# Optimization experiments

Hardware: AMD Instinct MI355X
Metric: run time of the kernel (lower is better)

Reference implementation:

```python
import jax, jax.numpy as jnp
import numpy as np

B, IN_CH, HID, H, W = 8, 64, 128, 128, 128
WS, NHEADS = 4, 4
HD = HID // NHEADS
GROUPS = 8  # min(8, hidden_ch)
EPS = 1e-5


def setup_inputs() -> dict:
    key = jax.random.key(0)
    ks = jax.random.split(key, 8)
    def w(k, shape):
        return jax.random.normal(k, shape, jnp.float32) * 0.02
    return {
        "x": jax.random.normal(ks[0], (B, IN_CH, H, W), jnp.float32),
        "h": jax.random.normal(ks[1], (B, HID, H, W), jnp.float32),
        "c": jax.random.normal(ks[2], (B, HID, H, W), jnp.float32),
        "Wproj": w(ks[3], (HID, IN_CH + HID)),
        "bproj": jnp.zeros((HID,), jnp.float32),
        "ln_g": jnp.ones((HID,), jnp.float32),
        "ln_b": jnp.zeros((HID,), jnp.float32),
        "Wqkv": w(ks[4], (3 * HID, HID)),
        "bqkv": jnp.zeros((3 * HID,), jnp.float32),
        "Wo": w(ks[5], (HID, HID)),
        "bo": jnp.zeros((HID,), jnp.float32),
        "Wgates": w(ks[6], (4 * HID, HID)),
        "bgates": jnp.zeros((4 * HID,), jnp.float32),
        "gn_g": jnp.ones((HID,), jnp.float32),
        "gn_b": jnp.zeros((HID,), jnp.float32),
    }


def group_norm(x, g, b):
    # x: [B, C, H, W], normalize per (group, spatial)
    Bx, C, Hx, Wx = x.shape
    xg = x.reshape(Bx, GROUPS, C // GROUPS, Hx, Wx)
    mu = xg.mean(axis=(2, 3, 4), keepdims=True)
    var = xg.var(axis=(2, 3, 4), keepdims=True)
    xn = ((xg - mu) * jax.lax.rsqrt(var + EPS)).reshape(Bx, C, Hx, Wx)
    return xn * g[:, None, None] + b[:, None, None]


def reference(x, h, c, Wproj, bproj, ln_g, ln_b, Wqkv, bqkv, Wo, bo,
              Wgates, bgates, gn_g, gn_b):
    # 1x1 conv input projection on concat(x, h)
    comb = jnp.concatenate([x, h], axis=1)  # [B, in+hid, H, W]
    proj = jnp.einsum('bihw,oi->bohw', comb, Wproj) + bproj[:, None, None]

    # window partition (H, W divisible by WS -> no padding)
    nh, nw = H // WS, W // WS
    xw = proj.reshape(B, HID, nh, WS, nw, WS)
    xw = xw.transpose(0, 2, 4, 3, 5, 1).reshape(B * nh * nw, WS * WS, HID)

    # LocalWindowAttention: LayerNorm -> QKV -> MHSA -> proj
    mu = xw.mean(axis=-1, keepdims=True)
    var = xw.var(axis=-1, keepdims=True)
    xn = (xw - mu) * jax.lax.rsqrt(var + EPS) * ln_g + ln_b
    qkv = (xn @ Wqkv.T + bqkv).reshape(-1, WS * WS, 3, NHEADS, HD)
    q = qkv[:, :, 0].transpose(0, 2, 1, 3)  # [Bw, nh, N, hd]
    k = qkv[:, :, 1].transpose(0, 2, 1, 3)
    v = qkv[:, :, 2].transpose(0, 2, 1, 3)
    scale = HD ** -0.5
    attn = jax.nn.softmax(jnp.einsum('whnd,whmd->whnm', q, k) * scale, axis=-1)
    out = jnp.einsum('whnm,whmd->whnd', attn, v)
    out = out.transpose(0, 2, 1, 3).reshape(-1, WS * WS, HID)
    out = out @ Wo.T + bo

    # window unpartition -> [B, C, H, W]
    attn_map = out.reshape(B, nh, nw, WS, WS, HID)
    attn_map = attn_map.transpose(0, 5, 1, 3, 2, 4).reshape(B, HID, H, W)
    attn_map = group_norm(attn_map, gn_g, gn_b)

    # conv-gated LSTM update (1x1 conv gates)
    gates = jnp.einsum('bchw,oc->bohw', attn_map, Wgates) + bgates[:, None, None]
    ci, cf, co, cg = jnp.split(gates, 4, axis=1)
    i = jax.nn.sigmoid(ci)
    f = jax.nn.sigmoid(cf)
    o = jax.nn.sigmoid(co)
    g = jnp.tanh(cg)
    cnext = f * c + i * g
    hnext = group_norm(o * jnp.tanh(cnext), gn_g, gn_b)
    return hnext, cnext
```

## Files before the change

### kernel.cpp

```cpp
#include <hip/hip_runtime.h>
#include <math.h>

typedef unsigned int uint;
typedef unsigned short ushort;
typedef short s16x8 __attribute__((ext_vector_type(8)));
typedef float f32x4 __attribute__((ext_vector_type(4)));

#define PIX 16384
#define EPSF 1e-5f

__device__ __forceinline__ ushort f2bf(float f) {
  union { float f; uint u; } v; v.f = f;
  uint u = v.u;
  uint r = (u + 0x7FFFu + ((u >> 16) & 1u)) >> 16;
  return (ushort)r;
}
__device__ __forceinline__ float bf2f(ushort h) {
  union { uint u; float f; } v; v.u = ((uint)h) << 16;
  return v.f;
}
__device__ __forceinline__ uint pk2(float a, float b) {
  return (uint)f2bf(a) | ((uint)f2bf(b) << 16);
}
__device__ __forceinline__ float fsigmoid(float v) { return 1.f / (1.f + __expf(-v)); }
__device__ __forceinline__ float ftanh(float v) { return 1.f - 2.f / (__expf(2.f * v) + 1.f); }

union Frag { uint4 u4; uint u[4]; s16x8 s; };

__global__ void k_prep(const float* __restrict__ Wp, const float* __restrict__ Wq,
                       const float* __restrict__ Wo, const float* __restrict__ Wg,
                       const float* __restrict__ ln_g,
                       ushort* __restrict__ FWp, ushort* __restrict__ FWq,
                       ushort* __restrict__ FWo, ushort* __restrict__ FWg) {
  int idx = blockIdx.x * 256 + threadIdx.x;
  const float* W; ushort* F; int KS, ldw, rel; bool scale = false;
  if (idx < 3072)       { W = Wp; F = FWp; KS = 6; ldw = 192; rel = idx; }
  else if (idx < 9216)  { W = Wq; F = FWq; KS = 4; ldw = 128; rel = idx - 3072; scale = true; }
  else if (idx < 11264) { W = Wo; F = FWo; KS = 4; ldw = 128; rel = idx - 9216; }
  else                  { W = Wg; F = FWg; KS = 4; ldw = 128; rel = idx - 11264; }
  int l = rel & 63, rest = rel >> 6;
  int ks = rest % KS, mt = rest / KS;
  int col = ks * 32 + (l >> 4) * 8;
  const float* src = W + (size_t)(mt * 16 + (l & 15)) * ldw + col;
  float g[8] = {1.f, 1.f, 1.f, 1.f, 1.f, 1.f, 1.f, 1.f};
  if (scale) {
    #pragma unroll
    for (int j = 0; j < 8; j++) g[j] = ln_g[col + j];
  }
  uint4 v;
  v.x = pk2(src[0] * g[0], src[1] * g[1]);
  v.y = pk2(src[2] * g[2], src[3] * g[3]);
  v.z = pk2(src[4] * g[4], src[5] * g[5]);
  v.w = pk2(src[6] * g[6], src[7] * g[7]);
  *reinterpret_cast<uint4*>(F + (size_t)rel * 8) = v;
}

__global__ void k_prep2(const float* __restrict__ Wq, const float* __restrict__ ln_g,
                        const float* __restrict__ ln_b, const float* __restrict__ bqkv,
                        float* __restrict__ Sarr, float* __restrict__ Tbarr) {
  int o = threadIdx.x;
  if (o >= 384) return;
  float S = 0.f, T = 0.f;
  const float* wr = Wq + (size_t)o * 128;
  for (int i = 0; i < 128; i++) {
    float wv = wr[i];
    S = fmaf(wv, ln_g[i], S);
    T = fmaf(wv, ln_b[i], T);
  }
  Sarr[o] = S;
  Tbarr[o] = T + bqkv[o];
}

__global__ __launch_bounds__(256, 3) void k_attn(
    const float* __restrict__ x, const float* __restrict__ h,
    const ushort* __restrict__ FWp, const float* __restrict__ bproj,
    const ushort* __restrict__ FWq, const float* __restrict__ Sarr,
    const float* __restrict__ Tbarr,
    const ushort* __restrict__ FWoT, const float* __restrict__ bo,
    ushort* __restrict__ attn_map, float* __restrict__ stA_raw)
{
  __shared__ __align__(16) char LM[51200];
  __shared__ float sSum[64], sSum2[64];
  __shared__ float sStat[16];

  const int t = threadIdx.x;
  const int bid = blockIdx.x;
  const int b = bid >> 8, wh = (bid >> 3) & 31, ww0 = bid & 7;
  const int w = t >> 6, l = t & 63, q = l >> 4, r16 = l & 15;

  uint* sInP = (uint*)LM;
  ushort* sXn = (ushort*)LM;

  if (t < 64) { sSum[t] = 0.f; sSum2[t] = 0.f; }
  if (t < 16) sStat[t] = 0.f;

  {
    const float* xb = x + (size_t)b * 64 * PIX;
    const float* hb = h + (size_t)b * 128 * PIX;
    #pragma unroll
    for (int it = 0; it < 6; it++) {
      int item = it * 256 + t;
      int wv = item & 3, r = (item >> 2) & 3, chp = item >> 4;
      int ch0 = chp * 2;
      int gpix = (wh * 4 + r) * 128 + ww0 * 16 + wv * 4;
      float4 a, c2;
      if (ch0 < 64) {
        a  = *reinterpret_cast<const float4*>(xb + (size_t)ch0 * PIX + gpix);
        c2 = *reinterpret_cast<const float4*>(xb + (size_t)(ch0 + 1) * PIX + gpix);
      } else {
        a  = *reinterpret_cast<const float4*>(hb + (size_t)(ch0 - 64) * PIX + gpix);
        c2 = *reinterpret_cast<const float4*>(hb + (size_t)(ch0 - 63) * PIX + gpix);
      }
      uint4 pkd;
      pkd.x = pk2(a.x, c2.x); pkd.y = pk2(a.y, c2.y);
      pkd.z = pk2(a.z, c2.z); pkd.w = pk2(a.w, c2.w);
      *reinterpret_cast<uint4*>(sInP + chp * 68 + wv * 16 + r * 4) = pkd;
    }
  }
  __syncthreads();

  f32x4 acc1[2][4];
  {
    #pragma unroll
    for (int mi = 0; mi < 2; mi++)
      #pragma unroll
      for (int nt = 0; nt < 4; nt++) acc1[mi][nt] = (f32x4){0.f, 0.f, 0.f, 0.f};
    for (int ks = 0; ks < 6; ks++) {
      Frag bf[4];
      #pragma unroll
      for (int nt = 0; nt < 4; nt++)
        #pragma unroll
        for (int s = 0; s < 4; s++)
          bf[nt].u[s] = sInP[(ks * 16 + q * 4 + s) * 68 + nt * 16 + r16];
      #pragma unroll
      for (int mi = 0; mi < 2; mi++) {
        Frag af;
        af.u4 = *reinterpret_cast<const uint4*>(FWp + (((w + mi * 4) * 6 + ks) * 64 + l) * 8);
        #pragma unroll
        for (int nt = 0; nt < 4; nt++)
          acc1[mi][nt] = __builtin_amdgcn_mfma_f32_16x16x32_bf16(af.s, bf[nt].s, acc1[mi][nt], 0, 0, 0);
      }
    }
  }
  __syncthreads();

  {
    float pst[4] = {0.f, 0.f, 0.f, 0.f}, pst2[4] = {0.f, 0.f, 0.f, 0.f};
    #pragma unroll
    for (int mi = 0; mi < 2; mi++) {
      int o0 = (w + mi * 4) * 16 + q * 4;
      const float4 bv = *reinterpret_cast<const float4*>(bproj + o0);
      #pragma unroll
      for (int nt = 0; nt < 4; nt++) {
        float v0 = acc1[mi][nt][0] + bv.x, v1 = acc1[mi][nt][1] + bv.y;
        float v2 = acc1[mi][nt][2] + bv.z, v3 = acc1[mi][nt][3] + bv.w;
        uint2 pk; pk.x = pk2(v0, v1); pk.y = pk2(v2, v3);
        *reinterpret_cast<uint2*>(sXn + (nt * 16 + r16) * 136 + o0) = pk;
        pst[nt]  += v0 + v1 + v2 + v3;
        pst2[nt] += v0 * v0 + v1 * v1 + v2 * v2 + v3 * v3;
      }
    }
    #pragma unroll
    for (int nt = 0; nt < 4; nt++) {
      float s = pst[nt], s2 = pst2[nt];
      s  += __shfl_xor(s, 16);  s  += __shfl_xor(s, 32);
      s2 += __shfl_xor(s2, 16); s2 += __shfl_xor(s2, 32);
      if (q == 0) {
        atomicAdd(&sSum[nt * 16 + r16], s);
        atomicAdd(&sSum2[nt * 16 + r16], s2);
      }
    }
  }
  __syncthreads();

  float rstd_[4], mr_[4];
  f32x4 accV[2][4];
  {
    Frag bfh[4][4];
    #pragma unroll
    for (int ks = 0; ks < 4; ks++)
      #pragma unroll
      for (int nt = 0; nt < 4; nt++)
        bfh[ks][nt].u4 = *reinterpret_cast<const uint4*>(sXn + (nt * 16 + r16) * 136 + ks * 32 + q * 8);

    #pragma unroll
    for (int nt = 0; nt < 4; nt++) {
      int tok = nt * 16 + r16;
      float mu = sSum[tok] * 0.0078125f;
      float var = sSum2[tok] * 0.0078125f - mu * mu;
      rstd_[nt] = rsqrtf(var + EPSF);
      mr_[nt] = -mu * rstd_[nt];
    }

    ushort* sQKu = (ushort*)(LM + 17408);
    #pragma unroll
    for (int mi = 0; mi < 4; mi++) {
      int mt = w + mi * 4;
      f32x4 accq[4];
      #pragma unroll
      for (int nt = 0; nt < 4; nt++) accq[nt] = (f32x4){0.f, 0.f, 0.f, 0.f};
      #pragma unroll
      for (int ks = 0; ks < 4; ks++) {
        Frag af;
        af.u4 = *reinterpret_cast<const uint4*>(FWq + ((mt * 4 + ks) * 64 + l) * 8);
        #pragma unroll
        for (int nt = 0; nt < 4; nt++)
          accq[nt] = __builtin_amdgcn_mfma_f32_16x16x32_bf16(af.s, bfh[ks][nt].s, accq[nt], 0, 0, 0);
      }
      int oo = mt * 16 + q * 4;
      const float4 S4  = *reinterpret_cast<const float4*>(Sarr + oo);
      const float4 Tb4 = *reinterpret_cast<const float4*>(Tbarr + oo);
      #pragma unroll
      for (int nt = 0; nt < 4; nt++) {
        float v0 = fmaf(rstd_[nt], accq[nt][0], fmaf(mr_[nt], S4.x, Tb4.x));
        float v1 = fmaf(rstd_[nt], accq[nt][1], fmaf(mr_[nt], S4.y, Tb4.y));
        float v2 = fmaf(rstd_[nt], accq[nt][2], fmaf(mr_[nt], S4.z, Tb4.z));
        float v3 = fmaf(rstd_[nt], accq[nt][3], fmaf(mr_[nt], S4.w, Tb4.w));
        uint2 pk; pk.x = pk2(v0, v1); pk.y = pk2(v2, v3);
        *reinterpret_cast<uint2*>(sQKu + nt * 4224 + r16 * 264 + oo) = pk;
      }
    }
    #pragma unroll
    for (int mi = 0; mi < 2; mi++) {
      int mt = w + 16 + mi * 4;
      #pragma unroll
      for (int nt = 0; nt < 4; nt++) accV[mi][nt] = (f32x4){0.f, 0.f, 0.f, 0.f};
      #pragma unroll
      for (int ks = 0; ks < 4; ks++) {
        Frag af;
        af.u4 = *reinterpret_cast<const uint4*>(FWq + ((mt * 4 + ks) * 64 + l) * 8);
        #pragma unroll
        for (int nt = 0; nt < 4; nt++)
          accV[mi][nt] = __builtin_amdgcn_mfma_f32_16x16x32_bf16(af.s, bfh[ks][nt].s, accV[mi][nt], 0, 0, 0);
      }
    }
  }
  __syncthreads();

  {
    ushort* sVu = (ushort*)LM;
    #pragma unroll
    for (int mi = 0; mi < 2; mi++) {
      int mt = w + 16 + mi * 4;
      int oo = mt * 16 + q * 4;
      const float4 S4  = *reinterpret_cast<const float4*>(Sarr + oo);
      const float4 Tb4 = *reinterpret_cast<const float4*>(Tbarr + oo);
      #pragma unroll
      for (int nt = 0; nt < 4; nt++) {
        float v0 = fmaf(rstd_[nt], accV[mi][nt][0], fmaf(mr_[nt], S4.x, Tb4.x));
        float v1 = fmaf(rstd_[nt], accV[mi][nt][1], fmaf(mr_[nt], S4.y, Tb4.y));
        float v2 = fmaf(rstd_[nt], accV[mi][nt][2], fmaf(mr_[nt], S4.z, Tb4.z));
        float v3 = fmaf(rstd_[nt], accV[mi][nt][3], fmaf(mr_[nt], S4.w, Tb4.w));
        ushort* vd = sVu + nt * 2048 + (oo - 256) * 16 + r16;
        vd[0] = f2bf(v0); vd[16] = f2bf(v1); vd[32] = f2bf(v2); vd[48] = f2bf(v3);
      }
    }
  }
  __syncthreads();

  {
    const float scale = 0.17677669529663687f;
    ushort* sQKw = (ushort*)(LM + 17408 + w * 8448);
    ushort* sPw  = sQKw;
    Frag af4[4], bf4[4];
    #pragma unroll
    for (int hd = 0; hd < 4; hd++) {
      af4[hd].u4 = *reinterpret_cast<const uint4*>(sQKw + r16 * 264 + hd * 32 + q * 8);
      bf4[hd].u4 = *reinterpret_cast<const uint4*>(sQKw + r16 * 264 + 128 + hd * 32 + q * 8);
    }
    #pragma unroll
    for (int hd = 0; hd < 4; hd++) {
      if (l < 32) {
        int row = l >> 1, hz = l & 1;
        uint4 z = {0u, 0u, 0u, 0u};
        *reinterpret_cast<uint4*>(sPw + hd * 512 + row * 32 + 16 + hz * 8) = z;
      }
    }
    f32x4 sc[4];
    #pragma unroll
    for (int hd = 0; hd < 4; hd++) {
      f32x4 z4 = (f32x4){0.f, 0.f, 0.f, 0.f};
      sc[hd] = __builtin_amdgcn_mfma_f32_16x16x32_bf16(af4[hd].s, bf4[hd].s, z4, 0, 0, 0);
    }
    #pragma unroll
    for (int hd = 0; hd < 4; hd++) {
      ushort* pd = sPw + hd * 512 + (q * 4) * 32 + r16;
      #pragma unroll
      for (int r = 0; r < 4; r++) {
        float sv = sc[hd][r] * scale;
        float mx = sv;
        mx = fmaxf(mx, __shfl_xor(mx, 1));
        mx = fmaxf(mx, __shfl_xor(mx, 2));
        mx = fmaxf(mx, __shfl_xor(mx, 4));
        mx = fmaxf(mx, __shfl_xor(mx, 8));
        float e = __expf(sv - mx);
        float sm = e;
        sm += __shfl_xor(sm, 1); sm += __shfl_xor(sm, 2);
        sm += __shfl_xor(sm, 4); sm += __shfl_xor(sm, 8);
        pd[r * 32] = f2bf(e / sm);
      }
    }
    ushort* sOw = sQKw + 2048;
    ushort* sVw = (ushort*)LM + w * 2048;
    #pragma unroll
    for (int hd = 0; hd < 4; hd++) {
      Frag pa;
      pa.u4 = *reinterpret_cast<const uint4*>(sPw + hd * 512 + r16 * 32 + q * 8);
      #pragma unroll
      for (int nt2 = 0; nt2 < 2; nt2++) {
        int ch = hd * 32 + nt2 * 16 + r16;
        int off = (q < 2) ? q * 8 : 0;
        Frag vf;
        vf.u4 = *reinterpret_cast<const uint4*>(sVw + ch * 16 + off);
        f32x4 z4 = (f32x4){0.f, 0.f, 0.f, 0.f};
        f32x4 o4 = __builtin_amdgcn_mfma_f32_16x16x32_bf16(pa.s, vf.s, z4, 0, 0, 0);
        ushort* od = sOw + (q * 4) * 136 + ch;
        od[0] = f2bf(o4[0]); od[136] = f2bf(o4[1]);
        od[272] = f2bf(o4[2]); od[408] = f2bf(o4[3]);
      }
    }
  }
  __syncthreads();

  {
    ushort* sFinu = (ushort*)LM;
    Frag a4[4][4];
    #pragma unroll
    for (int nt = 0; nt < 4; nt++) {
      ushort* sOnt = (ushort*)(LM + 17408 + nt * 8448 + 4096);
      #pragma unroll
      for (int ks = 0; ks < 4; ks++)
        a4[nt][ks].u4 = *reinterpret_cast<const uint4*>(sOnt + r16 * 136 + ks * 32 + q * 8);
    }
    #pragma unroll
    for (int mi2 = 0; mi2 < 2; mi2++) {
      int ntg = w + mi2 * 4;
      f32x4 acw[4];
      #pragma unroll
      for (int nt = 0; nt < 4; nt++) acw[nt] = (f32x4){0.f, 0.f, 0.f, 0.f};
      #pragma unroll
      for (int ks = 0; ks < 4; ks++) {
        Frag bfw;
        bfw.u4 = *reinterpret_cast<const uint4*>(FWoT + ((ntg * 4 + ks) * 64 + l) * 8);
        #pragma unroll
        for (int nt = 0; nt < 4; nt++)
          acw[nt] = __builtin_amdgcn_mfma_f32_16x16x32_bf16(a4[nt][ks].s, bfw.s, acw[nt], 0, 0, 0);
      }
      int ch = ntg * 16 + r16;
      float bb = bo[ch];
      #pragma unroll
      for (int nt = 0; nt < 4; nt++) {
        uint2 pk;
        pk.x = pk2(acw[nt][0] + bb, acw[nt][1] + bb);
        pk.y = pk2(acw[nt][2] + bb, acw[nt][3] + bb);
        *reinterpret_cast<uint2*>(sFinu + nt * 2048 + ch * 16 + q * 4) = pk;
      }
    }
  }
  __syncthreads();

  {
    ushort* sFinu = (ushort*)LM;
    #pragma unroll
    for (int it = 0; it < 4; it++) {
      int seg = it * 256 + t;
      int ch = seg >> 3, r = (seg >> 1) & 3, half = seg & 1;
      const ushort* f0 = sFinu + (half * 2    ) * 2048;
      const ushort* f1 = sFinu + (half * 2 + 1) * 2048;
      uint2 a  = *reinterpret_cast<const uint2*>(f0 + ch * 16 + r * 4);
      uint2 c2 = *reinterpret_cast<const uint2*>(f1 + ch * 16 + r * 4);
      uint4 val = {a.x, a.y, c2.x, c2.y};
      *reinterpret_cast<uint4*>(attn_map + (size_t)(b * 128 + ch) * PIX
                                + (wh * 4 + r) * 128 + ww0 * 16 + half * 8) = val;
      float sv = 0.f, sv2 = 0.f;
      uint uu[4] = {val.x, val.y, val.z, val.w};
      #pragma unroll
      for (int k2 = 0; k2 < 4; k2++) {
        float fv0 = bf2f((ushort)(uu[k2] & 0xFFFFu));
        float fv1 = bf2f((ushort)(uu[k2] >> 16));
        sv += fv0 + fv1; sv2 += fv0 * fv0 + fv1 * fv1;
      }
      sv  += __shfl_xor(sv, 1);  sv  += __shfl_xor(sv, 2);  sv  += __shfl_xor(sv, 4);
      sv2 += __shfl_xor(sv2, 1); sv2 += __shfl_xor(sv2, 2); sv2 += __shfl_xor(sv2, 4);
      if ((t & 7) == 0) {
        int g = ch >> 4;
        atomicAdd(&sStat[g * 2], sv);
        atomicAdd(&sStat[g * 2 + 1], sv2);
      }
    }
  }
  __syncthreads();
  if (t < 16) atomicAdd(&stA_raw[b * 16 + t], sStat[t]);
}

__global__ __launch_bounds__(256, 4) void k_gates(
    const ushort* __restrict__ attn_map, const float* __restrict__ stA_raw,
    const float* __restrict__ gn_g, const float* __restrict__ gn_b,
    const ushort* __restrict__ FWg, const float* __restrict__ bgates,
    const float* __restrict__ c, float* __restrict__ cnext,
    ushort* __restrict__ tbuf, float* __restrict__ stB_raw)
{
  __shared__ uint sG2[32 * 66];
  __shared__ float sA[128], sB[128];
  __shared__ float sStat[16];
  const int t = threadIdx.x, bid = blockIdx.x;
  const int b = bid >> 9, p0 = (bid & 511) * 32;
  const int w = t >> 6, l = t & 63, q = l >> 4, r16 = l & 15;

  if (t < 128) {
    int g = t >> 4;
    const float invN = 1.f / 262144.f;
    float mu = stA_raw[b * 16 + g * 2] * invN;
    float var = stA_raw[b * 16 + g * 2 + 1] * invN - mu * mu;
    float rs = rsqrtf(var + EPSF);
    float A = rs * gn_g[t];
    sA[t] = A; sB[t] = gn_b[t] - mu * A;
  }
  if (t >= 240) sStat[t - 240] = 0.f;
  __syncthreads();

  {
    int pr = t >> 2, px0 = (t & 3) * 8;
    int c0 = pr * 2;
    const ushort* ab = attn_map + (size_t)(b * 128) * PIX + p0 + px0;
    uint4 a0 = *reinterpret_cast<const uint4*>(ab + (size_t)c0 * PIX);
    uint4 a1 = *reinterpret_cast<const uint4*>(ab + (size_t)(c0 + 1) * PIX);
    float A0 = sA[c0], B0 = sB[c0], A1 = sA[c0 + 1], B1 = sB[c0 + 1];
    uint u0[4] = {a0.x, a0.y, a0.z, a0.w};
    uint u1[4] = {a1.x, a1.y, a1.z, a1.w};
    #pragma unroll
    for (int j = 0; j < 4; j++) {
      float v0lo = bf2f((ushort)(u0[j] & 0xFFFFu)) * A0 + B0;
      float v0hi = bf2f((ushort)(u0[j] >> 16)) * A0 + B0;
      float v1lo = bf2f((ushort)(u1[j] & 0xFFFFu)) * A1 + B1;
      float v1hi = bf2f((ushort)(u1[j] >> 16)) * A1 + B1;
      sG2[(px0 + 2 * j) * 66 + pr]     = pk2(v0lo, v1lo);
      sG2[(px0 + 2 * j + 1) * 66 + pr] = pk2(v0hi, v1hi);
    }
  }

  float4 cv[2][2];
  #pragma unroll
  for (int j = 0; j < 2; j++) {
    int ch = (w + 4 * j) * 16 + r16;
    const float* cb = c + (size_t)(b * 128 + ch) * PIX + p0 + q * 4;
    cv[j][0] = *reinterpret_cast<const float4*>(cb);
    cv[j][1] = *reinterpret_cast<const float4*>(cb + 16);
  }
  __syncthreads();

  f32x4 acc[4][2][2];
  #pragma unroll
  for (int g2 = 0; g2 < 4; g2++)
    #pragma unroll
    for (int j = 0; j < 2; j++)
      #pragma unroll
      for (int pxt = 0; pxt < 2; pxt++) acc[g2][j][pxt] = (f32x4){0.f, 0.f, 0.f, 0.f};

  const ushort* sGu = (const ushort*)sG2;
  for (int ks = 0; ks < 4; ks++) {
    Frag af[2];
    #pragma unroll
    for (int pxt = 0; pxt < 2; pxt++)
      af[pxt].u4 = *reinterpret_cast<const uint4*>(sGu + (pxt * 16 + r16) * 132 + ks * 32 + q * 8);
    #pragma unroll
    for (int g2 = 0; g2 < 4; g2++) {
      #pragma unroll
      for (int j = 0; j < 2; j++) {
        int ct = w + 4 * j + 8 * g2;
        Frag bfw;
        bfw.u4 = *reinterpret_cast<const uint4*>(FWg + ((ct * 4 + ks) * 64 + l) * 8);
        #pragma unroll
        for (int pxt = 0; pxt < 2; pxt++)
          acc[g2][j][pxt] = __builtin_amdgcn_mfma_f32_16x16x32_bf16(af[pxt].s, bfw.s, acc[g2][j][pxt], 0, 0, 0);
      }
    }
  }

  float gs[2] = {0.f, 0.f}, gs2[2] = {0.f, 0.f};
  #pragma unroll
  for (int j = 0; j < 2; j++) {
    int ch = (w + 4 * j) * 16 + r16;
    float bi = bgates[ch], bff = bgates[128 + ch], bog = bgates[256 + ch], bgg = bgates[384 + ch];
    #pragma unroll
    for (int pxt = 0; pxt < 2; pxt++) {
      size_t gbase = (size_t)(b * 128 + ch) * PIX + p0 + pxt * 16 + q * 4;
      const float cc[4] = {cv[j][pxt].x, cv[j][pxt].y, cv[j][pxt].z, cv[j][pxt].w};
      float cn[4], tv[4];
      #pragma unroll
      for (int r = 0; r < 4; r++) {
        float ig = fsigmoid(acc[0][j][pxt][r] + bi);
        float fg = fsigmoid(acc[1][j][pxt][r] + bff);
        float og = fsigmoid(acc[2][j][pxt][r] + bog);
        float gg = ftanh   (acc[3][j][pxt][r] + bgg);
        cn[r] = fg * cc[r] + ig * gg;
        tv[r] = og * ftanh(cn[r]);
        gs[j] += tv[r]; gs2[j] += tv[r] * tv[r];
      }
      float4 cno = {cn[0], cn[1], cn[2], cn[3]};
      *reinterpret_cast<float4*>(cnext + gbase) = cno;
      uint2 tpk;
      tpk.x = pk2(tv[0], tv[1]); tpk.y = pk2(tv[2], tv[3]);
      *reinterpret_cast<uint2*>(tbuf + gbase) = tpk;
    }
  }
  #pragma unroll
  for (int j = 0; j < 2; j++) {
    float s = gs[j], s2 = gs2[j];
    s += __shfl_xor(s, 1); s += __shfl_xor(s, 2); s += __shfl_xor(s, 4);
    s += __shfl_xor(s, 8); s += __shfl_xor(s, 16); s += __shfl_xor(s, 32);
    s2 += __shfl_xor(s2, 1); s2 += __shfl_xor(s2, 2); s2 += __shfl_xor(s2, 4);
    s2 += __shfl_xor(s2, 8); s2 += __shfl_xor(s2, 16); s2 += __shfl_xor(s2, 32);
    if (l == 0) {
      int g = w + 4 * j;
      atomicAdd(&sStat[g * 2], s);
      atomicAdd(&sStat[g * 2 + 1], s2);
    }
  }
  __syncthreads();
  if (t < 16) atomicAdd(&stB_raw[b * 16 + t], sStat[t]);
}

__global__ __launch_bounds__(256) void k_gnout(
    const ushort* __restrict__ tbuf, const float* __restrict__ stB_raw,
    const float* __restrict__ gn_g, const float* __restrict__ gn_b,
    float* __restrict__ hnext)
{
  size_t idx = ((size_t)blockIdx.x * 256 + threadIdx.x) * 8;
  if (idx >= (size_t)16777216) return;
  int chrow = (int)(idx >> 14);
  int b = chrow >> 7, ch = chrow & 127, g = ch >> 4;
  const float invN = 1.f / 262144.f;
  float mu = stB_raw[b * 16 + g * 2] * invN;
  float var = stB_raw[b * 16 + g * 2 + 1] * invN - mu * mu;
  float rstd = rsqrtf(var + EPSF);
  float A = gn_g[ch] * rstd, Bv = gn_b[ch] - mu * A;
  uint4 u = *reinterpret_cast<const uint4*>(tbuf + idx);
  float4 o0, o1;
  o0.x = bf2f((ushort)(u.x & 0xFFFFu)) * A + Bv;
  o0.y = bf2f((ushort)(u.x >> 16)) * A + Bv;
  o0.z = bf2f((ushort)(u.y & 0xFFFFu)) * A + Bv;
  o0.w = bf2f((ushort)(u.y >> 16)) * A + Bv;
  o1.x = bf2f((ushort)(u.z & 0xFFFFu)) * A + Bv;
  o1.y = bf2f((ushort)(u.z >> 16)) * A + Bv;
  o1.z = bf2f((ushort)(u.w & 0xFFFFu)) * A + Bv;
  o1.w = bf2f((ushort)(u.w >> 16)) * A + Bv;
  *reinterpret_cast<float4*>(hnext + idx) = o0;
  *reinterpret_cast<float4*>(hnext + idx + 4) = o1;
}

extern "C" void kernel_launch(void* const* d_in, const int* in_sizes, int n_in,
                              void* d_out, int out_size, void* d_ws, size_t ws_size,
                              hipStream_t stream) {
  (void)in_sizes; (void)n_in; (void)out_size; (void)ws_size;
  const float* x      = (const float*)d_in[0];
  const float* h      = (const float*)d_in[1];
  const float* c      = (const float*)d_in[2];
  const float* Wproj  = (const float*)d_in[3];
  const float* bproj  = (const float*)d_in[4];
  const float* ln_g   = (const float*)d_in[5];
  const float* ln_b   = (const float*)d_in[6];
  const float* Wqkv   = (const float*)d_in[7];
  const float* bqkv   = (const float*)d_in[8];
  const float* Wo     = (const float*)d_in[9];
  const float* bo     = (const float*)d_in[10];
  const float* Wgates = (const float*)d_in[11];
  const float* bgates = (const float*)d_in[12];
  const float* gn_g   = (const float*)d_in[13];
  const float* gn_b   = (const float*)d_in[14];

  float* out = (float*)d_out;
  float* hnext = out;
  float* cnext = out + 16777216;

  char* W = (char*)d_ws;
  ushort* attn = (ushort*)W;
  ushort* tbuf = (ushort*)(W + 33554432);
  size_t off = 67108864;
  ushort* FWp = (ushort*)(W + off); off += 49152;
  ushort* FWq = (ushort*)(W + off); off += 98304;
  ushort* FWo = (ushort*)(W + off); off += 32768;
  ushort* FWg = (ushort*)(W + off); off += 131072;
  float* stA_raw = (float*)(W + off); off += 512;
  float* stB_raw = (float*)(W + off); off += 512;
  float* Sarr    = (float*)(W + off); off += 1536;
  float* Tbarr   = (float*)(W + off); off += 1536;

  hipMemsetAsync(stA_raw, 0, 1024, stream);

  k_prep<<<76, 256, 0, stream>>>(Wproj, Wqkv, Wo, Wgates, ln_g, FWp, FWq, FWo, FWg);
  k_prep2<<<1, 384, 0, stream>>>(Wqkv, ln_g, ln_b, bqkv, Sarr, Tbarr);

  k_attn<<<2048, 256, 0, stream>>>(x, h, FWp, bproj, FWq, Sarr, Tbarr,
                                   FWo, bo, attn, stA_raw);
  k_gates<<<4096, 256, 0, stream>>>(attn, stA_raw, gn_g, gn_b, FWg, bgates,
                                    c, cnext, tbuf, stB_raw);
  k_gnout<<<8192, 256, 0, stream>>>(tbuf, stB_raw, gn_g, gn_b, hnext);
}
```

Baseline: 215.3 us.

## Split gates kernel across two blocks per pixel tile by channel half

Each k_gates block now handles only half of the output channel groups for a 32-pixel tile, doubling the grid to 8192 blocks and halving per-thread accumulators. The c-state load is hoisted before the first barrier to overlap with stat setup, and launch bounds are raised to allow more resident blocks. The cost is that each block redundantly loads and normalizes the full attn_map tile into shared memory, doubling that read traffic, and issues twice as many global stat atomics.

```diff
diff --git a/kernel.cpp b/kernel.cpp
--- a/kernel.cpp
+++ b/kernel.cpp
@@ -393,7 +393,7 @@
   if (t < 16) atomicAdd(&stA_raw[b * 16 + t], sStat[t]);
 }
 
-__global__ __launch_bounds__(256, 4) void k_gates(
+__global__ __launch_bounds__(256, 5) void k_gates(
     const ushort* __restrict__ attn_map, const float* __restrict__ stA_raw,
     const float* __restrict__ gn_g, const float* __restrict__ gn_b,
     const ushort* __restrict__ FWg, const float* __restrict__ bgates,
@@ -404,8 +404,11 @@
   __shared__ float sA[128], sB[128];
   __shared__ float sStat[16];
   const int t = threadIdx.x, bid = blockIdx.x;
-  const int b = bid >> 9, p0 = (bid & 511) * 32;
+  const int b = bid >> 10;
+  const int p0 = ((bid >> 1) & 511) * 32;
+  const int half = bid & 1;
   const int w = t >> 6, l = t & 63, q = l >> 4, r16 = l & 15;
+  const int oct = w + 4 * half;
 
   if (t < 128) {
     int g = t >> 4;
@@ -417,14 +420,22 @@
     sA[t] = A; sB[t] = gn_b[t] - mu * A;
   }
   if (t >= 240) sStat[t - 240] = 0.f;
+
+  float4 cv[2];
+  {
+    int ch = oct * 16 + r16;
+    const float* cb = c + (size_t)(b * 128 + ch) * PIX + p0 + q * 4;
+    cv[0] = *reinterpret_cast<const float4*>(cb);
+    cv[1] = *reinterpret_cast<const float4*>(cb + 16);
+  }
   __syncthreads();
 
   {
     int pr = t >> 2, px0 = (t & 3) * 8;
     int c0 = pr * 2;
-    const ushort* ab = attn_map + (size_t)(b * 128) * PIX + p0 + px0;
-    uint4 a0 = *reinterpret_cast<const uint4*>(ab + (size_t)c0 * PIX);
-    uint4 a1 = *reinterpret_cast<const uint4*>(ab + (size_t)(c0 + 1) * PIX);
+    const ushort* ab = attn_map + (size_t)(b * 128 + c0) * PIX + p0 + px0;
+    uint4 a0 = *reinterpret_cast<const uint4*>(ab);
+    uint4 a1 = *reinterpret_cast<const uint4*>(ab + PIX);
     float A0 = sA[c0], B0 = sB[c0], A1 = sA[c0 + 1], B1 = sB[c0 + 1];
     uint u0[4] = {a0.x, a0.y, a0.z, a0.w};
     uint u1[4] = {a1.x, a1.y, a1.z, a1.w};
@@ -438,24 +449,13 @@
       sG2[(px0 + 2 * j + 1) * 66 + pr] = pk2(v0hi, v1hi);
     }
   }
-
-  float4 cv[2][2];
-  #pragma unroll
-  for (int j = 0; j < 2; j++) {
-    int ch = (w + 4 * j) * 16 + r16;
-    const float* cb = c + (size_t)(b * 128 + ch) * PIX + p0 + q * 4;
-    cv[j][0] = *reinterpret_cast<const float4*>(cb);
-    cv[j][1] = *reinterpret_cast<const float4*>(cb + 16);
-  }
-  __syncthreads();
-
-  f32x4 acc[4][2][2];
+  __syncthreads();
+
+  f32x4 acc[4][2];
   #pragma unroll
   for (int g2 = 0; g2 < 4; g2++)
     #pragma unroll
-    for (int j = 0; j < 2; j++)
-      #pragma unroll
-      for (int pxt = 0; pxt < 2; pxt++) acc[g2][j][pxt] = (f32x4){0.f, 0.f, 0.f, 0.f};
+    for (int pxt = 0; pxt < 2; pxt++) acc[g2][pxt] = (f32x4){0.f, 0.f, 0.f, 0.f};
 
   const ushort* sGu = (const ushort*)sG2;
   for (int ks = 0; ks < 4; ks++) {
@@ -465,37 +465,33 @@
       af[pxt].u4 = *reinterpret_cast<const uint4*>(sGu + (pxt * 16 + r16) * 132 + ks * 32 + q * 8);
     #pragma unroll
     for (int g2 = 0; g2 < 4; g2++) {
-      #pragma unroll
-      for (int j = 0; j < 2; j++) {
-        int ct = w + 4 * j + 8 * g2;
-        Frag bfw;
-        bfw.u4 = *reinterpret_cast<const uint4*>(FWg + ((ct * 4 + ks) * 64 + l) * 8);
-        #pragma unroll
-        for (int pxt = 0; pxt < 2; pxt++)
-          acc[g2][j][pxt] = __builtin_amdgcn_mfma_f32_16x16x32_bf16(af[pxt].s, bfw.s, acc[g2][j][pxt], 0, 0, 0);
-      }
-    }
-  }
-
-  float gs[2] = {0.f, 0.f}, gs2[2] = {0.f, 0.f};
-  #pragma unroll
-  for (int j = 0; j < 2; j++) {
-    int ch = (w + 4 * j) * 16 + r16;
+      int ct = oct + 8 * g2;
+      Frag bfw;
+      bfw.u4 = *reinterpret_cast<const uint4*>(FWg + ((ct * 4 + ks) * 64 + l) * 8);
+      #pragma unroll
+      for (int pxt = 0; pxt < 2; pxt++)
+        acc[g2][pxt] = __builtin_amdgcn_mfma_f32_16x16x32_bf16(af[pxt].s, bfw.s, acc[g2][pxt], 0, 0, 0);
+    }
+  }
+
+  float gs = 0.f, gsq = 0.f;
+  {
+    int ch = oct * 16 + r16;
     float bi = bgates[ch], bff = bgates[128 + ch], bog = bgates[256 + ch], bgg = bgates[384 + ch];
     #pragma unroll
     for (int pxt = 0; pxt < 2; pxt++) {
       size_t gbase = (size_t)(b * 128 + ch) * PIX + p0 + pxt * 16 + q * 4;
-      const float cc[4] = {cv[j][pxt].x, cv[j][pxt].y, cv[j][pxt].z, cv[j][pxt].w};
+      const float cc[4] = {cv[pxt].x, cv[pxt].y, cv[pxt].z, cv[pxt].w};
       float cn[4], tv[4];
       #pragma unroll
       for (int r = 0; r < 4; r++) {
-        float ig = fsigmoid(acc[0][j][pxt][r] + bi);
-        float fg = fsigmoid(acc[1][j][pxt][r] + bff);
-        float og = fsigmoid(acc[2][j][pxt][r] + bog);
-        float gg = ftanh   (acc[3][j][pxt][r] + bgg);
+        float ig = fsigmoid(acc[0][pxt][r] + bi);
+        float fg = fsigmoid(acc[1][pxt][r] + bff);
+        float og = fsigmoid(acc[2][pxt][r] + bog);
+        float gg = ftanh   (acc[3][pxt][r] + bgg);
         cn[r] = fg * cc[r] + ig * gg;
         tv[r] = og * ftanh(cn[r]);
-        gs[j] += tv[r]; gs2[j] += tv[r] * tv[r];
+        gs += tv[r]; gsq += tv[r] * tv[r];
       }
       float4 cno = {cn[0], cn[1], cn[2], cn[3]};
       *reinterpret_cast<float4*>(cnext + gbase) = cno;
@@ -504,17 +500,15 @@
       *reinterpret_cast<uint2*>(tbuf + gbase) = tpk;
     }
   }
-  #pragma unroll
-  for (int j = 0; j < 2; j++) {
-    float s = gs[j], s2 = gs2[j];
+  {
+    float s = gs, s2 = gsq;
     s += __shfl_xor(s, 1); s += __shfl_xor(s, 2); s += __shfl_xor(s, 4);
     s += __shfl_xor(s, 8); s += __shfl_xor(s, 16); s += __shfl_xor(s, 32);
     s2 += __shfl_xor(s2, 1); s2 += __shfl_xor(s2, 2); s2 += __shfl_xor(s2, 4);
     s2 += __shfl_xor(s2, 8); s2 += __shfl_xor(s2, 16); s2 += __shfl_xor(s2, 32);
     if (l == 0) {
-      int g = w + 4 * j;
-      atomicAdd(&sStat[g * 2], s);
-      atomicAdd(&sStat[g * 2 + 1], s2);
+      atomicAdd(&sStat[oct * 2], s);
+      atomicAdd(&sStat[oct * 2 + 1], s2);
     }
   }
   __syncthreads();
@@ -593,7 +587,7 @@
 
   k_attn<<<2048, 256, 0, stream>>>(x, h, FWp, bproj, FWq, Sarr, Tbarr,
                                    FWo, bo, attn, stA_raw);
-  k_gates<<<4096, 256, 0, stream>>>(attn, stA_raw, gn_g, gn_b, FWg, bgates,
+  k_gates<<<8192, 256, 0, stream>>>(attn, stA_raw, gn_g, gn_b, FWg, bgates,
                                     c, cnext, tbuf, stB_raw);
   k_gnout<<<8192, 256, 0, stream>>>(tbuf, stB_raw, gn_g, gn_b, hnext);
 }
```

Result: slower. 221.0 us (+2.7%).
